# Optimization experiments

Measured on AMD Instinct MI355X. Metric: run time of the kernel, lower is better.

## Reference

```python
import jax, jax.numpy as jnp
import numpy as np

HEAD_DIM = 128
INFTY_APPROX = 1e+30
ROTARY_BASE = 10000.0

B, T, M = 2, 2048, 1024
H = M // HEAD_DIM  # 8


def setup_inputs() -> dict:
    key = jax.random.key(0)
    ks = jax.random.split(key, 5)
    x = jax.random.normal(ks[0], (B, T, M), dtype=jnp.float32)
    # mu-param inits: wq zeros in the original; use small random here for a
    # non-degenerate numerical baseline, scaled like kv_init = d_model**-0.5
    scale = M ** (-0.5)
    wq = jax.random.normal(ks[1], (M, H, HEAD_DIM), dtype=jnp.float32) * scale
    wk = jax.random.normal(ks[2], (M, H, HEAD_DIM), dtype=jnp.float32) * scale
    wv = jax.random.normal(ks[3], (M, H, HEAD_DIM), dtype=jnp.float32) * scale
    wo = jax.random.normal(ks[4], (H, HEAD_DIM, M), dtype=jnp.float32) * scale
    return {"x": x, "wq": wq, "wk": wk, "wv": wv, "wo": wo}


def _rotary(x, base=ROTARY_BASE):
    # x: [..., T, W]; non-interpretable RoPE over even/odd halves of W
    length, width = x.shape[-2], x.shape[-1]
    half = width // 2
    positions = jnp.arange(length)[:, None].astype(x.dtype)          # [T,1]
    ang_freqs = jnp.power(base, -jnp.arange(half) / half)[None, :]   # [1,half]
    radians = positions * ang_freqs                                  # [T,half]
    cos = jnp.cos(radians).astype(x.dtype)
    sin = jnp.sin(radians).astype(x.dtype)
    even, odd = jnp.split(x, 2, axis=-1)
    return jnp.concatenate([even * cos - odd * sin,
                            even * sin + odd * cos], axis=-1)


def _fractional_rotary(x):
    # rotary on first half of head dim, passthrough on the rest
    rot, skip = jnp.split(x, 2, axis=-1)
    return jnp.concatenate([_rotary(rot), skip], axis=-1)


def reference(x, wq, wk, wv, wo):
    q = jnp.einsum('bim,mhd->bhid', x, wq)
    k = jnp.einsum('bim,mhd->bhid', x, wk)
    v = jnp.einsum('bim,mhd->bhid', x, wv)
    q = _fractional_rotary(q)
    k = _fractional_rotary(k)
    # mu-param attention: scale by 1/HEAD_DIM (not 1/sqrt(D))
    s = jnp.einsum('bhid,bhjd->bhij', q, k) / HEAD_DIM
    i = jnp.arange(T)[:, None]
    j = jnp.arange(T)[None, :]
    mask = (i < j).astype(s.dtype)  # strictly-upper-triangular
    s = s - jnp.asarray(INFTY_APPROX, dtype=s.dtype) * mask
    p = jax.nn.softmax(s, axis=-1)
    o = jnp.einsum('bhij,bhjd->bhid', p, v)
    r = jnp.einsum('bhid,hdm->bim', o, wo)
    return r
```

## Files before the change

kernel.cpp:

```cpp
#include <hip/hip_runtime.h>

#define T_SEQ 2048
#define MDL   1024
#define NH    8
#define HD    128
#define SPLIT 4

typedef __bf16 bf16;
typedef __bf16 bf16x8 __attribute__((ext_vector_type(8)));
typedef __bf16 bf16x4 __attribute__((ext_vector_type(4)));
typedef float  f32x4  __attribute__((ext_vector_type(4)));

#define GLB(p) ((const __attribute__((address_space(1))) void*)(p))
#define LDS(p) ((__attribute__((address_space(3))) void*)(p))

#if __has_builtin(__builtin_amdgcn_exp2f)
#define EXP2(x) __builtin_amdgcn_exp2f(x)
#else
#define EXP2(x) __expf((x) * 0.6931471805599453f)
#endif

#define QSCALE 0.011271055f


__global__ __launch_bounds__(256) void prep_kernel(
    const float* __restrict__ x,
    const float* __restrict__ wq, const float* __restrict__ wk,
    const float* __restrict__ wv, const float* __restrict__ wo,
    bf16* __restrict__ xb, bf16* __restrict__ Wt, bf16* __restrict__ Wot)
{
    __shared__ bf16 t_lds[64 * 72];
    const int tid = threadIdx.x;
    if (blockIdx.x < 2048) {
        size_t i = ((size_t)blockIdx.x * 256 + tid) * 8;
        float4 v0 = *(const float4*)(x + i);
        float4 v1 = *(const float4*)(x + i + 4);
        bf16x8 o;
        o[0]=(bf16)v0.x; o[1]=(bf16)v0.y; o[2]=(bf16)v0.z; o[3]=(bf16)v0.w;
        o[4]=(bf16)v1.x; o[5]=(bf16)v1.y; o[6]=(bf16)v1.z; o[7]=(bf16)v1.w;
        *(bf16x8*)(xb + i) = o;
        return;
    }
    const int bx = blockIdx.x - 2048;
    const int sec = bx >> 8;
    const int tile = bx & 255;
    const int k0 = (tile >> 4) * 64, n0 = (tile & 15) * 64;
    const float* src = sec == 0 ? wq : sec == 1 ? wk : sec == 2 ? wv : wo;
    bf16* dst = sec < 3 ? (Wt + (size_t)sec * MDL * MDL) : Wot;

    const int ir = tid >> 2, jc = (tid & 3) * 16;
    const float* sp = src + (size_t)(k0 + ir) * MDL + n0 + jc;
    #pragma unroll
    for (int c = 0; c < 4; ++c) {
        float4 v = *(const float4*)(sp + c * 4);
        bf16x4 o; o[0]=(bf16)v.x; o[1]=(bf16)v.y; o[2]=(bf16)v.z; o[3]=(bf16)v.w;
        *(bf16x4*)&t_lds[ir * 72 + jc + c * 4] = o;
    }
    __syncthreads();
    bf16x8 o0, o1;
    #pragma unroll
    for (int jj = 0; jj < 8; ++jj) {
        o0[jj] = t_lds[(jc + jj) * 72 + ir];
        o1[jj] = t_lds[(jc + 8 + jj) * 72 + ir];
    }
    bf16* dp = dst + (size_t)(n0 + ir) * MDL + k0 + jc;
    *(bf16x8*)dp = o0;
    *(bf16x8*)(dp + 8) = o1;
}

__global__ __launch_bounds__(256) void qkv_rope_kernel(
    const bf16* __restrict__ xb, const bf16* __restrict__ Wt,
    bf16* __restrict__ Qb, bf16* __restrict__ Kt, bf16* __restrict__ Vt)
{
    __shared__ bf16 smem[32768];
    bf16* a_lds = smem;
    bf16* b_lds = smem + 16384;

    const int tid = threadIdx.x, bx = blockIdx.x;
    const int nt = bx % 24, mt = bx / 24;
    const int n0 = nt * 128, m0 = mt * 128;
    const int section = n0 >> 10;
    const int h = (n0 & 1023) >> 7;

    const int lane = tid & 63, w = tid >> 6;
    const int quad = lane >> 4, l15 = lane & 15;
    const int wr = w >> 1, wc = w & 1;
    const int srow = lane >> 3;

    const int csw = ((lane & 7) ^ srow) * 8;
    const bf16* gA = xb + (size_t)m0 * MDL + csw;
    const bf16* gB = Wt + (size_t)n0 * MDL + csw;

    f32x4 acc[4][4] = {};

    auto stage = [&](int k0, int buf) {
        #pragma unroll
        for (int i = 0; i < 4; ++i) {
            const int ch = w * 4 + i;
            const int row = ch * 8 + srow;
            __builtin_amdgcn_global_load_lds(GLB(gA + (size_t)row * MDL + k0),
                                             LDS(&a_lds[buf * 8192 + ch * 512]), 16, 0, 0);
            __builtin_amdgcn_global_load_lds(GLB(gB + (size_t)row * MDL + k0),
                                             LDS(&b_lds[buf * 8192 + ch * 512]), 16, 0, 0);
        }
    };

    auto compute = [&](int buf) {
        #pragma unroll
        for (int hh = 0; hh < 2; ++hh) {
            bf16x8 af[4], bfr[4];
            #pragma unroll
            for (int mi = 0; mi < 4; ++mi) {
                const int ra = wr * 64 + mi * 16 + l15;
                af[mi] = *(const bf16x8*)&a_lds[buf * 8192 + ra * 64 + ((hh * 4 + quad) ^ (ra & 7)) * 8];
            }
            #pragma unroll
            for (int ni = 0; ni < 4; ++ni) {
                const int rb = wc * 64 + ni * 16 + l15;
                bfr[ni] = *(const bf16x8*)&b_lds[buf * 8192 + rb * 64 + ((hh * 4 + quad) ^ (rb & 7)) * 8];
            }
            #pragma unroll
            for (int mi = 0; mi < 4; ++mi)
                #pragma unroll
                for (int ni = 0; ni < 4; ++ni)
                    acc[mi][ni] = __builtin_amdgcn_mfma_f32_16x16x32_bf16(af[mi], bfr[ni], acc[mi][ni], 0, 0, 0);
        }
    };

    stage(0, 0);
    __syncthreads();

    #pragma unroll 1
    for (int k0 = 0; k0 < MDL; k0 += 128) {
        stage(k0 + 64, 1);
        compute(0);
        __syncthreads();
        if (k0 + 128 < MDL) stage(k0 + 128, 0);
        compute(1);
        __syncthreads();
    }

    const int bdx = m0 >> 11;
    const int t0 = m0 & (T_SEQ - 1);
    const int bh = bdx * NH + h;

    if (section == 2) {
        #pragma unroll
        for (int c = 0; c < 2; ++c) {
            if (wc == c) {
                #pragma unroll
                for (int mi = 0; mi < 4; ++mi)
                    #pragma unroll
                    for (int r = 0; r < 4; ++r) {
                        int p = 16 * quad + 4 * r + mi;
                        int base = (wr * 8 + (p >> 3)) * 512 + (p & 7);
                        #pragma unroll
                        for (int ni = 0; ni < 4; ++ni)
                            smem[base + (ni * 16 + l15) * 8] = (bf16)acc[mi][ni][r];
                    }
            }
            __syncthreads();
            {
                const int t8 = tid >> 4;
                bf16* vp = Vt + ((size_t)(bh * 32 + (t0 >> 6) + (t8 >> 3))) * 8192
                              + (t8 & 7) * 1024 + c * 512 + (tid & 15) * 32;
                #pragma unroll
                for (int k = 0; k < 4; ++k)
                    *(bf16x8*)(vp + k * 8) = *(const bf16x8*)&smem[tid * 32 + k * 8];
            }
            __syncthreads();
        }
        return;
    }

    float fr_n[2];
    #pragma unroll
    for (int ni = 0; ni < 2; ++ni)
        fr_n[ni] = __expf(-(float)(ni * 16 + l15) * 0.28782313662425573f);

    if (section == 0) {
        #pragma unroll
        for (int mi = 0; mi < 4; ++mi) {
            #pragma unroll
            for (int r = 0; r < 4; ++r) {
                int t = t0 + wr * 64 + mi * 16 + quad * 4 + r;
                bf16* orow = Qb + ((size_t)bh * T_SEQ + t) * HD;
                if (wc == 0) {
                    #pragma unroll
                    for (int ni = 0; ni < 2; ++ni) {
                        int d = ni * 16 + l15;
                        float ang = (float)t * fr_n[ni];
                        float sn = __sinf(ang), cs = __cosf(ang);
                        float ev = acc[mi][ni][r];
                        float ov = acc[mi][ni + 2][r];
                        orow[d]      = (bf16)((ev * cs - ov * sn) * QSCALE);
                        orow[d + 32] = (bf16)((ev * sn + ov * cs) * QSCALE);
                    }
                } else {
                    #pragma unroll
                    for (int ni = 0; ni < 4; ++ni)
                        orow[64 + ni * 16 + l15] = (bf16)(acc[mi][ni][r] * QSCALE);
                }
            }
        }
    } else {
        #pragma unroll
        for (int c = 0; c < 2; ++c) {
            if (wr == c) {
                #pragma unroll
                for (int mi = 0; mi < 4; ++mi) {
                    #pragma unroll
                    for (int r = 0; r < 4; ++r) {
                        int tl = mi * 16 + quad * 4 + r;
                        int t = t0 + c * 64 + tl;
                        if (wc == 0) {
                            #pragma unroll
                            for (int ni = 0; ni < 2; ++ni) {
                                int d = ni * 16 + l15;
                                float ang = (float)t * fr_n[ni];
                                float sn = __sinf(ang), cs = __cosf(ang);
                                float ev = acc[mi][ni][r];
                                float ov = acc[mi][ni + 2][r];
                                smem[(d >> 3) * 512 + tl * 8 + (d & 7)] = (bf16)(ev * cs - ov * sn);
                                int d2 = d + 32;
                                smem[(d2 >> 3) * 512 + tl * 8 + (d2 & 7)] = (bf16)(ev * sn + ov * cs);
                            }
                        } else {
                            #pragma unroll
                            for (int ni = 0; ni < 4; ++ni) {
                                int d = 64 + ni * 16 + l15;
                                smem[(d >> 3) * 512 + tl * 8 + (d & 7)] = (bf16)acc[mi][ni][r];
                            }
                        }
                    }
                }
            }
            __syncthreads();
            {
                bf16* kp = Kt + ((size_t)(bh * 32 + (t0 >> 6) + c)) * 8192 + tid * 32;
                #pragma unroll
                for (int k = 0; k < 4; ++k)
                    *(bf16x8*)(kp + k * 8) = *(const bf16x8*)&smem[tid * 32 + k * 8];
            }
            __syncthreads();
        }
    }
}

__global__ __launch_bounds__(256) void attn_kernel(
    const bf16* __restrict__ Qb, const bf16* __restrict__ Kt,
    const bf16* __restrict__ Vt, bf16* __restrict__ PO, float* __restrict__ Pl)
{
    __shared__ bf16 k_lds[8192];
    __shared__ bf16 v_lds[8192];
    __shared__ bf16 p_lds[4][32 * 72];

    const int tid = threadIdx.x, lane = tid & 63, w = tid >> 6;
    const int quad = lane >> 4, l15 = lane & 15;
    const int bx = blockIdx.x;
    const int xcd  = bx & 7;
    const int slot = bx >> 3;
    const int bh   = xcd * 2 + (slot >> 5);
    const int s0   = slot & (SPLIT - 1);
    const int ip   = (slot >> 2) & 7;
    const int tA = 2 * ip + 2;

    const bf16* Kbh = Kt + (size_t)bh * 32 * 8192;
    const bf16* Vbh = Vt + (size_t)bh * 32 * 8192;

    bf16x8 kreg[4], vreg[4];
    bf16x8 qf[2][4];
    f32x4 Of[2][8];
    float l_r[2][4];

    auto fetch = [&](int g) {
        const int jt = (g < tA) ? g : g - tA;
        const bf16* kt = Kbh + (size_t)jt * 8192 + tid * 8;
        const bf16* vt = Vbh + (size_t)jt * 8192 + tid * 8;
        #pragma unroll
        for (int k = 0; k < 4; ++k) {
            kreg[k] = *(const bf16x8*)(kt + k * 2048);
            vreg[k] = *(const bf16x8*)(vt + k * 2048);
        }
    };

    fetch(s0);
    int pqt = -1;

    #pragma unroll 1
    for (int g = s0; g < 34; g += SPLIT) {
        const int ph = (g >= tA);
        const int qt = ph ? 15 - ip : ip;
        const int jt = ph ? g - tA : g;

        if (qt != pqt) {
            if (pqt >= 0) {
                const size_t slotq = ((size_t)bh * 16 + pqt) * SPLIT + s0;
                #pragma unroll
                for (int mi = 0; mi < 2; ++mi)
                    #pragma unroll
                    for (int r = 0; r < 4; ++r) {
                        float ls = l_r[mi][r];
                        ls += __shfl_xor(ls, 1); ls += __shfl_xor(ls, 2);
                        ls += __shfl_xor(ls, 4); ls += __shfl_xor(ls, 8);
                        const int row = w * 32 + mi * 16 + quad * 4 + r;
                        if (l15 == 0) Pl[slotq * 128 + row] = ls;
                        bf16* pr = PO + (slotq * 128 + row) * 128;
                        #pragma unroll
                        for (int di = 0; di < 8; ++di)
                            pr[di * 16 + l15] = (bf16)Of[mi][di][r];
                    }
            }
            #pragma unroll
            for (int mi = 0; mi < 2; ++mi) {
                const bf16* qrow = Qb + ((size_t)bh * T_SEQ + qt * 128 + w * 32 + mi * 16 + l15) * HD + quad * 8;
                #pragma unroll
                for (int kk = 0; kk < 4; ++kk)
                    qf[mi][kk] = *(const bf16x8*)(qrow + kk * 32);
                #pragma unroll
                for (int di = 0; di < 8; ++di) Of[mi][di] = (f32x4){0.f, 0.f, 0.f, 0.f};
                #pragma unroll
                for (int r = 0; r < 4; ++r) l_r[mi][r] = 0.f;
            }
            pqt = qt;
        }

        __syncthreads();
        #pragma unroll
        for (int k = 0; k < 4; ++k) {
            *(bf16x8*)&k_lds[k * 2048 + tid * 8] = kreg[k];
            *(bf16x8*)&v_lds[k * 2048 + tid * 8] = vreg[k];
        }
        if (g + SPLIT < 34) fetch(g + SPLIT);
        __syncthreads();

        f32x4 sa[2][4] = {};
        #pragma unroll
        for (int kk = 0; kk < 4; ++kk) {
            bf16x8 kb[4];
            #pragma unroll
            for (int ni = 0; ni < 4; ++ni)
                kb[ni] = *(const bf16x8*)&k_lds[(kk * 4 + quad) * 512 + (ni * 16 + l15) * 8];
            #pragma unroll
            for (int ni = 0; ni < 4; ++ni)
                #pragma unroll
                for (int mi = 0; mi < 2; ++mi)
                    sa[mi][ni] = __builtin_amdgcn_mfma_f32_16x16x32_bf16(qf[mi][kk], kb[ni], sa[mi][ni], 0, 0, 0);
        }

        const bool diag = (jt >= 2 * qt);
        #pragma unroll
        for (int mi = 0; mi < 2; ++mi) {
            const int rowb = w * 32 + mi * 16 + quad * 4;
            #pragma unroll
            for (int r = 0; r < 4; ++r) {
                float ps = 0.f;
                bf16x4 pq;
                #pragma unroll
                for (int ni = 0; ni < 4; ++ni) {
                    float pv = EXP2(sa[mi][ni][r]);
                    if (diag && (jt * 64 + ni * 16 + l15) > (qt * 128 + rowb + r)) pv = 0.f;
                    ps += pv;
                    pq[ni] = (bf16)pv;
                }
                *(bf16x4*)&p_lds[w][(mi * 16 + quad * 4 + r) * 72 + l15 * 4] = pq;
                l_r[mi][r] += ps;
            }
        }

        #pragma unroll
        for (int kk = 0; kk < 2; ++kk) {
            bf16x8 pa[2];
            #pragma unroll
            for (int mi = 0; mi < 2; ++mi)
                pa[mi] = *(const bf16x8*)&p_lds[w][(mi * 16 + l15) * 72 + kk * 32 + quad * 8];
            #pragma unroll
            for (int di = 0; di < 8; ++di) {
                bf16x8 vb = *(const bf16x8*)&v_lds[(kk * 4 + quad) * 1024 + (di * 16 + l15) * 8];
                #pragma unroll
                for (int mi = 0; mi < 2; ++mi)
                    Of[mi][di] = __builtin_amdgcn_mfma_f32_16x16x32_bf16(pa[mi], vb, Of[mi][di], 0, 0, 0);
            }
        }
    }

    {
        const size_t slotq = ((size_t)bh * 16 + pqt) * SPLIT + s0;
        #pragma unroll
        for (int mi = 0; mi < 2; ++mi)
            #pragma unroll
            for (int r = 0; r < 4; ++r) {
                float ls = l_r[mi][r];
                ls += __shfl_xor(ls, 1); ls += __shfl_xor(ls, 2);
                ls += __shfl_xor(ls, 4); ls += __shfl_xor(ls, 8);
                const int row = w * 32 + mi * 16 + quad * 4 + r;
                if (l15 == 0) Pl[slotq * 128 + row] = ls;
                bf16* pr = PO + (slotq * 128 + row) * 128;
                #pragma unroll
                for (int di = 0; di < 8; ++di)
                    pr[di * 16 + l15] = (bf16)Of[mi][di][r];
            }
    }
}

__global__ __launch_bounds__(256) void attn_combine_kernel(
    const bf16* __restrict__ PO, const float* __restrict__ Pl,
    bf16* __restrict__ Ob)
{
    const int idx = blockIdx.x * 256 + threadIdx.x;
    const int dcol = (idx & 15) * 8;
    const int rowg = idx >> 4;
    const int bh = rowg >> 11, qrow = rowg & 2047;
    const int qt = qrow >> 7, row = qrow & 127;
    const int ns = (2 * qt + 2 < SPLIT) ? (2 * qt + 2) : SPLIT;

    float acc[8] = {};
    float l = 0.f;
    for (int s = 0; s < ns; ++s) {
        const size_t base = (((size_t)bh * 16 + qt) * SPLIT + s) * 128 + row;
        bf16x8 po = *(const bf16x8*)&PO[base * 128 + dcol];
        #pragma unroll
        for (int jj = 0; jj < 8; ++jj) acc[jj] += (float)po[jj];
        l += Pl[base];
    }
    const float inv = 1.f / l;
    const int b = bh >> 3, hh = bh & 7, t = qt * 128 + row;
    bf16x8 o;
    #pragma unroll
    for (int jj = 0; jj < 8; ++jj) o[jj] = (bf16)(acc[jj] * inv);
    *(bf16x8*)(Ob + ((size_t)(b * T_SEQ + t) * NH + hh) * HD + dcol) = o;
}

__global__ __launch_bounds__(256) void out_proj_kernel(
    const bf16* __restrict__ Ob, const bf16* __restrict__ Wot,
    float* __restrict__ out)
{
    __shared__ bf16 a_lds[2][128 * 64];
    __shared__ bf16 b_lds[2][64 * 64];

    const int tid = threadIdx.x, bx = blockIdx.x;
    const int nt = bx & 15, mt = bx >> 4;
    const int n0 = nt * 64, m0 = mt * 128;

    const int lane = tid & 63, w = tid >> 6;
    const int quad = lane >> 4, l15 = lane & 15;
    const int wr = w >> 1, wc = w & 1;
    const int srow = lane >> 3;

    const int csw = ((lane & 7) ^ srow) * 8;
    const bf16* gA = Ob  + (size_t)m0 * MDL + csw;
    const bf16* gB = Wot + (size_t)n0 * MDL + csw;

    f32x4 acc[4][2] = {};

    auto stage = [&](int k0, int buf) {
        #pragma unroll
        for (int i = 0; i < 4; ++i) {
            const int ch = w * 4 + i;
            const int row = ch * 8 + srow;
            __builtin_amdgcn_global_load_lds(GLB(gA + (size_t)row * MDL + k0),
                                             LDS(&a_lds[buf][ch * 512]), 16, 0, 0);
        }
        #pragma unroll
        for (int i = 0; i < 2; ++i) {
            const int ch = w * 2 + i;
            const int row = ch * 8 + srow;
            __builtin_amdgcn_global_load_lds(GLB(gB + (size_t)row * MDL + k0),
                                             LDS(&b_lds[buf][ch * 512]), 16, 0, 0);
        }
    };

    auto compute = [&](int buf) {
        #pragma unroll
        for (int hh = 0; hh < 2; ++hh) {
            bf16x8 af[4], bfr[2];
            #pragma unroll
            for (int mi = 0; mi < 4; ++mi) {
                const int ra = wr * 64 + mi * 16 + l15;
                af[mi] = *(const bf16x8*)&a_lds[buf][ra * 64 + ((hh * 4 + quad) ^ (ra & 7)) * 8];
            }
            #pragma unroll
            for (int ni = 0; ni < 2; ++ni) {
                const int rb = wc * 32 + ni * 16 + l15;
                bfr[ni] = *(const bf16x8*)&b_lds[buf][rb * 64 + ((hh * 4 + quad) ^ (rb & 7)) * 8];
            }
            #pragma unroll
            for (int mi = 0; mi < 4; ++mi)
                #pragma unroll
                for (int ni = 0; ni < 2; ++ni)
                    acc[mi][ni] = __builtin_amdgcn_mfma_f32_16x16x32_bf16(af[mi], bfr[ni], acc[mi][ni], 0, 0, 0);
        }
    };

    stage(0, 0);
    __syncthreads();

    #pragma unroll 1
    for (int k0 = 0; k0 < MDL; k0 += 128) {
        stage(k0 + 64, 1);
        compute(0);
        __syncthreads();
        if (k0 + 128 < MDL) stage(k0 + 128, 0);
        compute(1);
        __syncthreads();
    }

    #pragma unroll
    for (int mi = 0; mi < 4; ++mi)
        #pragma unroll
        for (int r = 0; r < 4; ++r) {
            int row_g = m0 + wr * 64 + mi * 16 + quad * 4 + r;
            float* crow = out + (size_t)row_g * MDL + n0;
            #pragma unroll
            for (int ni = 0; ni < 2; ++ni)
                crow[wc * 32 + ni * 16 + l15] = acc[mi][ni][r];
        }
}

extern "C" void kernel_launch(void* const* d_in, const int* in_sizes, int n_in,
                              void* d_out, int out_size, void* d_ws, size_t ws_size,
                              hipStream_t stream) {
    const float* x  = (const float*)d_in[0];
    const float* wq = (const float*)d_in[1];
    const float* wk = (const float*)d_in[2];
    const float* wv = (const float*)d_in[3];
    const float* wo = (const float*)d_in[4];
    float* out = (float*)d_out;

    const size_t NTOK = (size_t)2 * NH * T_SEQ * HD;
    bf16*  Qb  = (bf16*)d_ws;
    bf16*  Kt  = Qb + NTOK;
    bf16*  Vt  = Kt + NTOK;
    bf16*  Ob  = Vt + NTOK;
    bf16*  Wot = Ob + NTOK;
    bf16*  PO  = Wot + (size_t)MDL * MDL;
    float* Pl  = (float*)(PO + (size_t)16 * 16 * SPLIT * 128 * 128);

    bf16* xbuf = (bf16*)d_out;
    bf16* Wt   = xbuf + (size_t)4096 * MDL;

    prep_kernel<<<3072, 256, 0, stream>>>(x, wq, wk, wv, wo, xbuf, Wt, Wot);
    qkv_rope_kernel<<<768, 256, 0, stream>>>(xbuf, Wt, Qb, Kt, Vt);
    attn_kernel<<<16 * 8 * SPLIT, 256, 0, stream>>>(Qb, Kt, Vt, PO, Pl);
    attn_combine_kernel<<<2048, 256, 0, stream>>>(PO, Pl, Ob);
    out_proj_kernel<<<512, 256, 0, stream>>>(Ob, Wot, out);
}
```

Baseline: 190.8 us.

## Fuse all five stages into one cooperative persistent kernel with grid syncs

Turns each stage into a device body function and runs them all in one cooperative mega kernel of 512 blocks, with grid-wide syncs between stages in place of separate kernel launches. The aim is to remove launch gaps and the tail drain between kernels. The cost is that every stage now runs at 512 blocks with one shared LDS footprint and a launch bound that may cap registers, and each grid sync carries overhead. If the cooperative launch fails, it falls back to the old five launches.

```diff
diff --git a/kernel.cpp b/kernel.cpp
--- a/kernel.cpp
+++ b/kernel.cpp
@@ -1,4 +1,7 @@
 #include <hip/hip_runtime.h>
+#include <hip/hip_cooperative_groups.h>
+
+namespace cg = cooperative_groups;
 
 #define T_SEQ 2048
 #define MDL   1024
@@ -23,16 +26,14 @@
 #define QSCALE 0.011271055f
 
 
-__global__ __launch_bounds__(256) void prep_kernel(
-    const float* __restrict__ x,
-    const float* __restrict__ wq, const float* __restrict__ wk,
-    const float* __restrict__ wv, const float* __restrict__ wo,
-    bf16* __restrict__ xb, bf16* __restrict__ Wt, bf16* __restrict__ Wot)
-{
-    __shared__ bf16 t_lds[64 * 72];
-    const int tid = threadIdx.x;
-    if (blockIdx.x < 2048) {
-        size_t i = ((size_t)blockIdx.x * 256 + tid) * 8;
+
+__device__ __forceinline__ void prep_body(
+    int vb, int tid, bf16* t_lds,
+    const float* x, const float* wq, const float* wk, const float* wv,
+    const float* wo, bf16* xb, bf16* Wt, bf16* Wot)
+{
+    if (vb < 2048) {
+        size_t i = ((size_t)vb * 256 + tid) * 8;
         float4 v0 = *(const float4*)(x + i);
         float4 v1 = *(const float4*)(x + i + 4);
         bf16x8 o;
@@ -41,7 +42,7 @@
         *(bf16x8*)(xb + i) = o;
         return;
     }
-    const int bx = blockIdx.x - 2048;
+    const int bx = vb - 2048;
     const int sec = bx >> 8;
     const int tile = bx & 255;
     const int k0 = (tile >> 4) * 64, n0 = (tile & 15) * 64;
@@ -50,6 +51,7 @@
 
     const int ir = tid >> 2, jc = (tid & 3) * 16;
     const float* sp = src + (size_t)(k0 + ir) * MDL + n0 + jc;
+    __syncthreads();
     #pragma unroll
     for (int c = 0; c < 4; ++c) {
         float4 v = *(const float4*)(sp + c * 4);
@@ -68,15 +70,14 @@
     *(bf16x8*)(dp + 8) = o1;
 }
 
-__global__ __launch_bounds__(256) void qkv_rope_kernel(
-    const bf16* __restrict__ xb, const bf16* __restrict__ Wt,
-    bf16* __restrict__ Qb, bf16* __restrict__ Kt, bf16* __restrict__ Vt)
-{
-    __shared__ bf16 smem[32768];
+__device__ __forceinline__ void qkv_body(
+    int bx, int tid, bf16* smem,
+    const bf16* xb, const bf16* Wt,
+    bf16* Qb, bf16* Kt, bf16* Vt)
+{
     bf16* a_lds = smem;
     bf16* b_lds = smem + 16384;
 
-    const int tid = threadIdx.x, bx = blockIdx.x;
     const int nt = bx % 24, mt = bx / 24;
     const int n0 = nt * 128, m0 = mt * 128;
     const int section = n0 >> 10;
@@ -127,6 +128,7 @@
         }
     };
 
+    __syncthreads();
     stage(0, 0);
     __syncthreads();
 
@@ -247,17 +249,17 @@
     }
 }
 
-__global__ __launch_bounds__(256) void attn_kernel(
-    const bf16* __restrict__ Qb, const bf16* __restrict__ Kt,
-    const bf16* __restrict__ Vt, bf16* __restrict__ PO, float* __restrict__ Pl)
-{
-    __shared__ bf16 k_lds[8192];
-    __shared__ bf16 v_lds[8192];
-    __shared__ bf16 p_lds[4][32 * 72];
-
-    const int tid = threadIdx.x, lane = tid & 63, w = tid >> 6;
+__device__ __forceinline__ void attn_body(
+    int bx, int tid, bf16* smem,
+    const bf16* Qb, const bf16* Kt, const bf16* Vt,
+    bf16* PO, float* Pl)
+{
+    bf16* k_lds = smem;
+    bf16* v_lds = smem + 8192;
+    const int lane = tid & 63, w = tid >> 6;
+    bf16* p_w = smem + 16384 + w * (32 * 72);
+
     const int quad = lane >> 4, l15 = lane & 15;
-    const int bx = blockIdx.x;
     const int xcd  = bx & 7;
     const int slot = bx >> 3;
     const int bh   = xcd * 2 + (slot >> 5);
@@ -363,7 +365,7 @@
                     ps += pv;
                     pq[ni] = (bf16)pv;
                 }
-                *(bf16x4*)&p_lds[w][(mi * 16 + quad * 4 + r) * 72 + l15 * 4] = pq;
+                *(bf16x4*)&p_w[(mi * 16 + quad * 4 + r) * 72 + l15 * 4] = pq;
                 l_r[mi][r] += ps;
             }
         }
@@ -373,7 +375,7 @@
             bf16x8 pa[2];
             #pragma unroll
             for (int mi = 0; mi < 2; ++mi)
-                pa[mi] = *(const bf16x8*)&p_lds[w][(mi * 16 + l15) * 72 + kk * 32 + quad * 8];
+                pa[mi] = *(const bf16x8*)&p_w[(mi * 16 + l15) * 72 + kk * 32 + quad * 8];
             #pragma unroll
             for (int di = 0; di < 8; ++di) {
                 bf16x8 vb = *(const bf16x8*)&v_lds[(kk * 4 + quad) * 1024 + (di * 16 + l15) * 8];
@@ -403,11 +405,9 @@
     }
 }
 
-__global__ __launch_bounds__(256) void attn_combine_kernel(
-    const bf16* __restrict__ PO, const float* __restrict__ Pl,
-    bf16* __restrict__ Ob)
-{
-    const int idx = blockIdx.x * 256 + threadIdx.x;
+__device__ __forceinline__ void combine_body(
+    int idx, const bf16* PO, const float* Pl, bf16* Ob)
+{
     const int dcol = (idx & 15) * 8;
     const int rowg = idx >> 4;
     const int bh = rowg >> 11, qrow = rowg & 2047;
@@ -431,14 +431,13 @@
     *(bf16x8*)(Ob + ((size_t)(b * T_SEQ + t) * NH + hh) * HD + dcol) = o;
 }
 
-__global__ __launch_bounds__(256) void out_proj_kernel(
-    const bf16* __restrict__ Ob, const bf16* __restrict__ Wot,
-    float* __restrict__ out)
-{
-    __shared__ bf16 a_lds[2][128 * 64];
-    __shared__ bf16 b_lds[2][64 * 64];
-
-    const int tid = threadIdx.x, bx = blockIdx.x;
+__device__ __forceinline__ void out_proj_body(
+    int bx, int tid, bf16* smem,
+    const bf16* Ob, const bf16* Wot, float* out)
+{
+    bf16* a_lds = smem;
+    bf16* b_lds = smem + 16384;
+
     const int nt = bx & 15, mt = bx >> 4;
     const int n0 = nt * 64, m0 = mt * 128;
 
@@ -459,14 +458,14 @@
             const int ch = w * 4 + i;
             const int row = ch * 8 + srow;
             __builtin_amdgcn_global_load_lds(GLB(gA + (size_t)row * MDL + k0),
-                                             LDS(&a_lds[buf][ch * 512]), 16, 0, 0);
+                                             LDS(&a_lds[buf * 8192 + ch * 512]), 16, 0, 0);
         }
         #pragma unroll
         for (int i = 0; i < 2; ++i) {
             const int ch = w * 2 + i;
             const int row = ch * 8 + srow;
             __builtin_amdgcn_global_load_lds(GLB(gB + (size_t)row * MDL + k0),
-                                             LDS(&b_lds[buf][ch * 512]), 16, 0, 0);
+                                             LDS(&b_lds[buf * 4096 + ch * 512]), 16, 0, 0);
         }
     };
 
@@ -477,12 +476,12 @@
             #pragma unroll
             for (int mi = 0; mi < 4; ++mi) {
                 const int ra = wr * 64 + mi * 16 + l15;
-                af[mi] = *(const bf16x8*)&a_lds[buf][ra * 64 + ((hh * 4 + quad) ^ (ra & 7)) * 8];
+                af[mi] = *(const bf16x8*)&a_lds[buf * 8192 + ra * 64 + ((hh * 4 + quad) ^ (ra & 7)) * 8];
             }
             #pragma unroll
             for (int ni = 0; ni < 2; ++ni) {
                 const int rb = wc * 32 + ni * 16 + l15;
-                bfr[ni] = *(const bf16x8*)&b_lds[buf][rb * 64 + ((hh * 4 + quad) ^ (rb & 7)) * 8];
+                bfr[ni] = *(const bf16x8*)&b_lds[buf * 4096 + rb * 64 + ((hh * 4 + quad) ^ (rb & 7)) * 8];
             }
             #pragma unroll
             for (int mi = 0; mi < 4; ++mi)
@@ -492,6 +491,7 @@
         }
     };
 
+    __syncthreads();
     stage(0, 0);
     __syncthreads();
 
@@ -515,6 +515,80 @@
             for (int ni = 0; ni < 2; ++ni)
                 crow[wc * 32 + ni * 16 + l15] = acc[mi][ni][r];
         }
+}
+
+__global__ __launch_bounds__(256, 2) void mega_kernel(
+    const float* __restrict__ x,  const float* __restrict__ wq,
+    const float* __restrict__ wk, const float* __restrict__ wv,
+    const float* __restrict__ wo,
+    bf16* xb, bf16* Wt, bf16* Wot,
+    bf16* Qb, bf16* Kt, bf16* Vt,
+    bf16* PO, float* Pl, bf16* Ob, float* out)
+{
+    __shared__ bf16 smem[32768];
+    const int tid = threadIdx.x, bid = blockIdx.x;
+    cg::grid_group grid = cg::this_grid();
+
+    #pragma unroll 1
+    for (int vb = bid; vb < 3072; vb += 512)
+        prep_body(vb, tid, smem, x, wq, wk, wv, wo, xb, Wt, Wot);
+    grid.sync();
+
+    #pragma unroll 1
+    for (int vb = bid; vb < 768; vb += 512)
+        qkv_body(vb, tid, smem, xb, Wt, Qb, Kt, Vt);
+    grid.sync();
+
+    attn_body(bid, tid, smem, Qb, Kt, Vt, PO, Pl);
+    grid.sync();
+
+    #pragma unroll 1
+    for (int vb = bid; vb < 2048; vb += 512)
+        combine_body(vb * 256 + tid, PO, Pl, Ob);
+    grid.sync();
+
+    out_proj_body(bid, tid, smem, Ob, Wot, out);
+}
+
+__global__ __launch_bounds__(256) void prep_kernel(
+    const float* __restrict__ x, const float* __restrict__ wq,
+    const float* __restrict__ wk, const float* __restrict__ wv,
+    const float* __restrict__ wo,
+    bf16* __restrict__ xb, bf16* __restrict__ Wt, bf16* __restrict__ Wot)
+{
+    __shared__ bf16 t_lds[64 * 72];
+    prep_body(blockIdx.x, threadIdx.x, t_lds, x, wq, wk, wv, wo, xb, Wt, Wot);
+}
+
+__global__ __launch_bounds__(256) void qkv_rope_kernel(
+    const bf16* __restrict__ xb, const bf16* __restrict__ Wt,
+    bf16* __restrict__ Qb, bf16* __restrict__ Kt, bf16* __restrict__ Vt)
+{
+    __shared__ bf16 smem[32768];
+    qkv_body(blockIdx.x, threadIdx.x, smem, xb, Wt, Qb, Kt, Vt);
+}
+
+__global__ __launch_bounds__(256) void attn_kernel(
+    const bf16* __restrict__ Qb, const bf16* __restrict__ Kt,
+    const bf16* __restrict__ Vt, bf16* __restrict__ PO, float* __restrict__ Pl)
+{
+    __shared__ bf16 smem[8192 + 8192 + 4 * 32 * 72];
+    attn_body(blockIdx.x, threadIdx.x, smem, Qb, Kt, Vt, PO, Pl);
+}
+
+__global__ __launch_bounds__(256) void attn_combine_kernel(
+    const bf16* __restrict__ PO, const float* __restrict__ Pl,
+    bf16* __restrict__ Ob)
+{
+    combine_body(blockIdx.x * 256 + threadIdx.x, PO, Pl, Ob);
+}
+
+__global__ __launch_bounds__(256) void out_proj_kernel(
+    const bf16* __restrict__ Ob, const bf16* __restrict__ Wot,
+    float* __restrict__ out)
+{
+    __shared__ bf16 smem[16384 + 8192];
+    out_proj_body(blockIdx.x, threadIdx.x, smem, Ob, Wot, out);
 }
 
 extern "C" void kernel_launch(void* const* d_in, const int* in_sizes, int n_in,
@@ -539,9 +613,27 @@
     bf16* xbuf = (bf16*)d_out;
     bf16* Wt   = xbuf + (size_t)4096 * MDL;
 
-    prep_kernel<<<3072, 256, 0, stream>>>(x, wq, wk, wv, wo, xbuf, Wt, Wot);
-    qkv_rope_kernel<<<768, 256, 0, stream>>>(xbuf, Wt, Qb, Kt, Vt);
-    attn_kernel<<<16 * 8 * SPLIT, 256, 0, stream>>>(Qb, Kt, Vt, PO, Pl);
-    attn_combine_kernel<<<2048, 256, 0, stream>>>(PO, Pl, Ob);
-    out_proj_kernel<<<512, 256, 0, stream>>>(Ob, Wot, out);
-}
+    int dev = 0;
+    (void)hipGetDevice(&dev);
+    int coop = 0;
+    (void)hipDeviceGetAttribute(&coop, hipDeviceAttributeCooperativeLaunch, dev);
+
+    hipError_t e = hipErrorUnknown;
+    if (coop) {
+        void* args[] = {
+            (void*)&x, (void*)&wq, (void*)&wk, (void*)&wv, (void*)&wo,
+            (void*)&xbuf, (void*)&Wt, (void*)&Wot,
+            (void*)&Qb, (void*)&Kt, (void*)&Vt,
+            (void*)&PO, (void*)&Pl, (void*)&Ob, (void*)&out };
+        e = hipLaunchCooperativeKernel((const void*)mega_kernel,
+                                       dim3(512), dim3(256), args, 0, stream);
+    }
+    if (e != hipSuccess) {
+        (void)hipGetLastError();
+        prep_kernel<<<3072, 256, 0, stream>>>(x, wq, wk, wv, wo, xbuf, Wt, Wot);
+        qkv_rope_kernel<<<768, 256, 0, stream>>>(xbuf, Wt, Qb, Kt, Vt);
+        attn_kernel<<<16 * 8 * SPLIT, 256, 0, stream>>>(Qb, Kt, Vt, PO, Pl);
+        attn_combine_kernel<<<2048, 256, 0, stream>>>(PO, Pl, Ob);
+        out_proj_kernel<<<512, 256, 0, stream>>>(Ob, Wot, out);
+    }
+}
```

After: 452.6 us. +137.2%, slower.
